# Kernel tuning notes

Measured on AMD Instinct MI355X. Metric: run time of the kernel, lower is better.

The kernel has to match this reference:

```python
import jax, jax.numpy as jnp
import numpy as np
from jax import lax

B, T, L = 16, 200, 250
IDIM, ODIM, DUNITS = 512, 80, 1024
ATT_DIM, ACONV_CHANS, ACONV_K = 128, 32, 31
PRENET = 256


def setup_inputs() -> dict:
    key = jax.random.key(0)
    ks = iter(jax.random.split(key, 40))
    def nrm(shape, fan_in):
        return jax.random.normal(next(ks), shape, jnp.float32) * (fan_in ** -0.5)
    inp = {}
    inp['hs'] = jax.random.normal(next(ks), (B, T, IDIM), jnp.float32)
    inp['hlens'] = jax.random.randint(next(ks), (B,), T // 2, T + 1)
    inp['ys'] = jax.random.normal(next(ks), (B, L, ODIM), jnp.float32)
    # location-aware attention params
    inp['W_enc'] = nrm((IDIM, ATT_DIM), IDIM)
    inp['b_enc'] = jnp.zeros((ATT_DIM,), jnp.float32)
    inp['W_dec'] = nrm((DUNITS, ATT_DIM), DUNITS)
    inp['W_att'] = nrm((ACONV_CHANS, ATT_DIM), ACONV_CHANS)
    inp['loc_conv_w'] = nrm((ACONV_CHANS, 1, ACONV_K), ACONV_K)
    inp['gvec_w'] = nrm((ATT_DIM,), ATT_DIM)
    inp['gvec_b'] = jnp.zeros((), jnp.float32)
    # prenet (no bias, dropout off in eval)
    inp['prenet_W1'] = nrm((ODIM, PRENET), ODIM)
    inp['prenet_W2'] = nrm((PRENET, PRENET), PRENET)
    # LSTM cells (torch gate order i,f,g,o; bih+bhh folded into one bias)
    in0 = IDIM + PRENET
    inp['Wih0'] = nrm((4 * DUNITS, in0), in0)
    inp['Whh0'] = nrm((4 * DUNITS, DUNITS), DUNITS)
    inp['b0'] = jnp.zeros((4 * DUNITS,), jnp.float32)
    inp['Wih1'] = nrm((4 * DUNITS, DUNITS), DUNITS)
    inp['Whh1'] = nrm((4 * DUNITS, DUNITS), DUNITS)
    inp['b1'] = jnp.zeros((4 * DUNITS,), jnp.float32)
    # output heads
    inp['feat_W'] = nrm((DUNITS, ODIM), DUNITS)
    inp['prob_W'] = nrm((DUNITS,), DUNITS)
    inp['prob_b'] = jnp.zeros((), jnp.float32)
    # postnet: conv(no bias) + BN(eval; running mean=0, var=1 folded away) + tanh
    inp['post_w_in'] = nrm((512, ODIM, 5), 5 * ODIM)
    inp['post_g_in'] = jnp.ones((512,), jnp.float32)
    inp['post_b_in'] = jnp.zeros((512,), jnp.float32)
    inp['post_w_mid'] = nrm((3, 512, 512, 5), 5 * 512)
    inp['post_g_mid'] = jnp.ones((3, 512), jnp.float32)
    inp['post_b_mid'] = jnp.zeros((3, 512), jnp.float32)
    inp['post_w_out'] = nrm((ODIM, 512, 5), 5 * 512)
    inp['post_g_out'] = jnp.ones((ODIM,), jnp.float32)
    inp['post_b_out'] = jnp.zeros((ODIM,), jnp.float32)
    return inp


def _conv1d(x, w, pad):
    # x: [B, Cin, T], w: [Cout, Cin, K]
    return lax.conv_general_dilated(x, w, (1,), [(pad, pad)],
                                    dimension_numbers=('NCH', 'OIH', 'NCH'))


def _lstm(x, h, c, Wih, Whh, b):
    g = x @ Wih.T + h @ Whh.T + b
    i, f, gg, o = jnp.split(g, 4, axis=-1)
    c2 = jax.nn.sigmoid(f) * c + jax.nn.sigmoid(i) * jnp.tanh(gg)
    return jax.nn.sigmoid(o) * jnp.tanh(c2), c2


def reference(hs, hlens, ys, W_enc, b_enc, W_dec, W_att, loc_conv_w, gvec_w, gvec_b,
              prenet_W1, prenet_W2, Wih0, Whh0, b0, Wih1, Whh1, b1,
              feat_W, prob_W, prob_b,
              post_w_in, post_g_in, post_b_in, post_w_mid, post_g_mid, post_b_mid,
              post_w_out, post_g_out, post_b_out):
    mask = jnp.arange(T)[None, :] < hlens[:, None]            # [B,T]
    pre_enc = hs @ W_enc + b_enc                              # [B,T,A] precomputed
    # teacher forcing: prenet input at step i is ys[:, i-1] (zeros at i=0);
    # prenet has no recurrent dependency -> vectorize over time
    prev = jnp.concatenate([jnp.zeros((B, 1, ODIM), hs.dtype), ys[:, :L - 1]], axis=1)
    pren = jax.nn.relu(jax.nn.relu(prev @ prenet_W1) @ prenet_W2)  # [B,L,256]
    att_w0 = mask.astype(hs.dtype) / hlens[:, None].astype(hs.dtype)
    z = jnp.zeros((B, DUNITS), hs.dtype)
    carry0 = (z, z, z, z, att_w0)

    def step(carry, pren_t):
        z0, c0, z1, c1, att_w = carry
        conv = _conv1d(att_w[:, None, :], loc_conv_w, ACONV_K // 2)   # [B,C,T]
        e = jnp.tanh(pre_enc + jnp.einsum('bct,ca->bta', conv, W_att)
                     + (z0 @ W_dec)[:, None, :]) @ gvec_w + gvec_b    # [B,T]
        e = jnp.where(mask, e, -1e30)
        w = jax.nn.softmax(2.0 * e, axis=1)                           # scaling=2.0
        att_c = jnp.einsum('bt,btd->bd', w, hs)
        x = jnp.concatenate([att_c, pren_t], axis=1)
        z0n, c0n = _lstm(x, z0, c0, Wih0, Whh0, b0)
        z1n, c1n = _lstm(z0n, z1, c1, Wih1, Whh1, b1)
        return (z0n, c0n, z1n, c1n, w), (z1n @ feat_W, z1n @ prob_W + prob_b)

    _, (outs, probs) = lax.scan(step, carry0, jnp.swapaxes(pren, 0, 1))
    outs = jnp.transpose(outs, (1, 2, 0))   # [B, odim, L] (matches torch.stack dim=2)
    probs = probs.T                         # [B, L]
    # postnet (BN in eval with running mean=0/var=1 reduces to gamma*x+beta)
    h = jnp.tanh(post_g_in[:, None] * _conv1d(outs, post_w_in, 2) + post_b_in[:, None])
    for i in range(3):
        h = jnp.tanh(post_g_mid[i][:, None] * _conv1d(h, post_w_mid[i], 2)
                     + post_b_mid[i][:, None])
    h = post_g_out[:, None] * _conv1d(h, post_w_out, 2) + post_b_out[:, None]
    post_outs = outs + h
    return jnp.swapaxes(post_outs, 1, 2), jnp.swapaxes(outs, 1, 2), probs
```

## Files before the change

### kernel.cpp

```cpp
#include <hip/hip_runtime.h>
#include <cstdint>
#include <cstddef>

constexpr int B_ = 16, T_ = 200, L_ = 250;
constexpr int IDIM = 512, ODIM = 80, DUNITS = 1024;
constexpr int ADIM = 128, ACH = 32, AK = 31;
constexpr int PRE = 256;
constexpr int TPAD = 208;

typedef _Float16 h16;
typedef _Float16 half8 __attribute__((ext_vector_type(8)));
typedef _Float16 half4 __attribute__((ext_vector_type(4)));
typedef float f32x4 __attribute__((ext_vector_type(4)));

constexpr int FSTEP = 800;
constexpr int FZ0W = 0, FDPW = 256, FAW = 288;

constexpr size_t OFF_PE    = 0;
constexpr size_t OFF_H0H   = 851968;
constexpr size_t OFF_Z1H   = 917504;
constexpr size_t OFF_ATTC  = 983040;
constexpr size_t OFF_DP    = 999424;
constexpr size_t OFF_FLAGS = 1007616;
constexpr size_t OFF_XT1   = 1807616;
constexpr size_t OFF_XTA   = 2888960;
constexpr size_t OFF_XTB   = 7214336;
constexpr size_t ZERO_BYTES= 11539712;
constexpr size_t OFF_MB    = 11539712;
constexpr size_t OFF_WDR   = 11547904;
constexpr size_t OFF_PREN  = 11810048;
constexpr size_t OFF_HSH   = 13858048;
constexpr size_t OFF_W0AH  = 17134848;
constexpr size_t OFF_WHH0  = 23426304;
constexpr size_t OFF_WI1   = 31814912;
constexpr size_t OFF_WHH1  = 40203520;
constexpr size_t OFF_Z1ALL = 48592128;
constexpr size_t OFF_WTIN  = 56784128;
constexpr size_t OFF_WTMID = 57439488;
constexpr size_t OFF_WTOUT = 65303808;
constexpr size_t OFF_PSC   = 65713408;

__device__ __forceinline__ float fsig(float x) {
  x = fminf(fmaxf(x, -30.f), 30.f);
  return __builtin_amdgcn_rcpf(1.f + __expf(-x));
}
__device__ __forceinline__ float ftanh(float x) {
  x = fminf(fmaxf(x, -15.f), 15.f);
  const float e = __expf(2.f * x);
  return (e - 1.f) * __builtin_amdgcn_rcpf(e + 1.f);
}
__device__ __forceinline__ f32x4 mfma16(half8 a, half8 b, f32x4 c) {
  return __builtin_amdgcn_mfma_f32_16x16x32_f16(a, b, c, 0, 0, 0);
}
__device__ __forceinline__ half8 load8_agent(const h16* p) {
  union { unsigned long long q[2]; half8 v; } cv;
  cv.q[0] = __hip_atomic_load((const unsigned long long*)p, __ATOMIC_RELAXED,
                              __HIP_MEMORY_SCOPE_AGENT);
  cv.q[1] = __hip_atomic_load(((const unsigned long long*)p) + 1, __ATOMIC_RELAXED,
                              __HIP_MEMORY_SCOPE_AGENT);
  return cv.v;
}
__device__ __forceinline__ float loadf_agent(const float* p) {
  union { unsigned u; float f; } cv;
  cv.u = __hip_atomic_load((const unsigned*)p, __ATOMIC_RELAXED,
                           __HIP_MEMORY_SCOPE_AGENT);
  return cv.f;
}
__device__ __forceinline__ void storef_agent(float* p, float v) {
  union { unsigned u; float f; } cv; cv.f = v;
  __hip_atomic_store((unsigned*)p, cv.u, __ATOMIC_RELAXED, __HIP_MEMORY_SCOPE_AGENT);
}
__device__ __forceinline__ int loadw(const int* p) {
  return __hip_atomic_load(p, __ATOMIC_RELAXED, __HIP_MEMORY_SCOPE_AGENT);
}
__device__ __forceinline__ void storew(int* p, int v) {
  __hip_atomic_store(p, v, __ATOMIC_RELAXED, __HIP_MEMORY_SCOPE_AGENT);
}
__device__ __forceinline__ void poll_n(const int* base, const int n) {
  if ((int)threadIdx.x < n) {
    const int* f = base + threadIdx.x;
    while (loadw(f) == 0) __builtin_amdgcn_s_sleep(1);
  }
  __syncthreads();
  __builtin_amdgcn_sched_barrier(0);
}
__device__ __forceinline__ void poll_all256(const int* base) {
  const int* f = base + threadIdx.x;
  while (loadw(f) == 0) __builtin_amdgcn_s_sleep(1);
  __syncthreads();
  __builtin_amdgcn_sched_barrier(0);
}


__global__ void k_zero(float4* __restrict__ p, int n4) {
  const int i = blockIdx.x * blockDim.x + threadIdx.x;
  if (i < n4) p[i] = make_float4(0.f, 0.f, 0.f, 0.f);
}

__global__ void __launch_bounds__(128) k_preenc(const float* __restrict__ hs,
    const float* __restrict__ W_enc, const float* __restrict__ b_enc,
    h16* __restrict__ pe_h) {
  const int bt = blockIdx.x, b = bt / T_, tt = bt % T_;
  __shared__ float s[IDIM];
  for (int i = threadIdx.x; i < IDIM; i += 128) s[i] = hs[(size_t)bt * IDIM + i];
  __syncthreads();
  const int a = threadIdx.x;
  float acc = b_enc[a];
#pragma unroll 4
  for (int d = 0; d < IDIM; ++d) acc += s[d] * W_enc[d * ADIM + a];
  pe_h[((size_t)b * ADIM + a) * TPAD + tt] = (h16)acc;
}

__global__ void k_precMb(const float* __restrict__ lconv, const float* __restrict__ W_att,
                         h16* __restrict__ Mb) {
  const int at = blockIdx.x, lane = threadIdx.x;
  const int a = at * 16 + (lane & 15);
  const int k0 = (lane >> 4) * 8;
  half8 o;
#pragma unroll
  for (int j = 0; j < 8; ++j) {
    const int k = k0 + j;
    float v = 0.f;
    if (k < AK)
      for (int c = 0; c < ACH; ++c) v += lconv[c * AK + k] * W_att[c * ADIM + a];
    o[j] = (h16)v;
  }
  *(half8*)(Mb + (size_t)(at * 64 + lane) * 8) = o;
}

__global__ void k_cvt_perm(const float* __restrict__ src, h16* __restrict__ dst,
                           const int K) {
  const int rr = blockIdx.x;
  const int u = rr >> 2, g = rr & 3;
  const float* s = src + (size_t)(g * 1024 + u) * K;
  h16* d = dst + (size_t)rr * K;
  for (int k = threadIdx.x; k < K; k += 256) d[k] = (h16)s[k];
}

__global__ void k_cvt_wdec(const float* __restrict__ Wdec, h16* __restrict__ Wdr) {
  const int a = blockIdx.x;
  for (int k = threadIdx.x; k < 1024; k += 256)
    Wdr[(size_t)a * 1024 + k] = (h16)Wdec[(size_t)k * ADIM + a];
}

__global__ void k_cvt_f32f16(const float* __restrict__ src, h16* __restrict__ dst) {
  const size_t i = ((size_t)blockIdx.x * 256 + threadIdx.x) * 4;
  const float4 v = *(const float4*)(src + i);
  half4 o; o[0] = (h16)v.x; o[1] = (h16)v.y; o[2] = (h16)v.z; o[3] = (h16)v.w;
  *(half4*)(dst + i) = o;
}

__global__ void k_prenet1(const float* __restrict__ ys, const float* __restrict__ W1,
                          float* __restrict__ h1) {
  const int bl = blockIdx.x, b = bl / L_, l = bl % L_;
  __shared__ float s[ODIM];
  if (threadIdx.x < ODIM)
    s[threadIdx.x] = (l == 0) ? 0.f : ys[((size_t)b * L_ + l - 1) * ODIM + threadIdx.x];
  __syncthreads();
  const int p = threadIdx.x;
  float acc = 0.f;
#pragma unroll 4
  for (int o = 0; o < ODIM; ++o) acc += s[o] * W1[o * PRE + p];
  h1[(size_t)bl * PRE + p] = fmaxf(acc, 0.f);
}

__global__ void k_prenet2h(const float* __restrict__ h1, const float* __restrict__ W2,
                           h16* __restrict__ pren_h) {
  const int bl = blockIdx.x, b = bl / L_, ll = bl % L_;
  __shared__ float s[PRE];
  s[threadIdx.x] = h1[(size_t)bl * PRE + threadIdx.x];
  __syncthreads();
  const int p = threadIdx.x;
  float acc = 0.f;
#pragma unroll 4
  for (int o = 0; o < PRE; ++o) acc += s[o] * W2[o * PRE + p];
  pren_h[((size_t)ll * B_ + b) * PRE + p] = (h16)fmaxf(acc, 0.f);
}

__global__ void k_cvt_wpin(const float* __restrict__ w, h16* __restrict__ o) {
  const int co = blockIdx.x;
  for (int i = threadIdx.x; i < 640; i += 256) {
    const int k = i >> 7, ci = i & 127;
    o[(size_t)co * 640 + i] = (ci < 80) ? (h16)w[((size_t)co * 80 + ci) * 5 + k] : (h16)0.f;
  }
}
__global__ void k_cvt_wpmid(const float* __restrict__ w, h16* __restrict__ o) {
  const int idx = blockIdx.x;
  const float* s = w + (size_t)idx * 512 * 5;
  h16* d = o + (size_t)idx * 2560;
  for (int i = threadIdx.x; i < 2560; i += 256) {
    const int k = i >> 9, ci = i & 511;
    d[i] = (h16)s[(size_t)ci * 5 + k];
  }
}
__global__ void k_cvt_wpout(const float* __restrict__ w, h16* __restrict__ o) {
  const int co = blockIdx.x;
  for (int i = threadIdx.x; i < 2560; i += 256) {
    const int k = i >> 9, ci = i & 511;
    o[(size_t)co * 2560 + i] = (h16)w[((size_t)co * 512 + ci) * 5 + k];
  }
}

template <int CIP, int NK, bool TANH, bool FINAL>
__global__ void __launch_bounds__(256) k_cvmf(const h16* __restrict__ xT,
    const h16* __restrict__ wT, const float* __restrict__ gamma,
    const float* __restrict__ beta, h16* __restrict__ yT,
    const float* __restrict__ res, float* __restrict__ out0) {
  __shared__ float s_red[4][64][5];
  __shared__ float s_g[16][20];
  constexpr int KTOT = NK * 128;
  const int b = blockIdx.x, l0 = blockIdx.y * 16, co0 = blockIdx.z * 16;
  const int tid = threadIdx.x, lane = tid & 63, wave = tid >> 6;
  const int nloc = lane & 15, kl8 = (lane >> 4) * 8;
  const h16* wr = wT + (size_t)(co0 + nloc) * KTOT + wave * (NK * 32) + kl8;
  half8 w[NK];
#pragma unroll
  for (int c = 0; c < NK; ++c) w[c] = *(const half8*)(wr + c * 32);
  f32x4 acc = {0.f, 0.f, 0.f, 0.f};
  const h16* xb = xT + (size_t)b * 264 * CIP;
#pragma unroll
  for (int c = 0; c < NK; ++c) {
    const int kg = wave * (NK * 32) + c * 32;
    const int k = kg / CIP, ci = kg & (CIP - 1);
    const half8 a = *(const half8*)(xb + (size_t)(l0 + nloc + k) * CIP + ci + kl8);
    acc = mfma16(a, w[c], acc);
  }
#pragma unroll
  for (int r = 0; r < 4; ++r) s_red[wave][lane][r] = acc[r];
  __syncthreads();
  {
    const float v = s_red[0][lane][wave] + s_red[1][lane][wave]
                  + s_red[2][lane][wave] + s_red[3][lane][wave];
    s_g[lane & 15][4 * (lane >> 4) + wave] = v;
  }
  __syncthreads();
  {
    const int co_l = tid & 15, l_l = tid >> 4;
    const int co = co0 + co_l, l = l0 + l_l;
    if (l < L_) {
      float v = gamma[co] * s_g[co_l][l_l] + beta[co];
      if (TANH) v = ftanh(v);
      if (FINAL) {
        const size_t o = ((size_t)b * L_ + l) * ODIM + co;
        out0[o] = res[o] + v;
      } else {
        yT[((size_t)b * 264 + l + 2) * 512 + co] = (h16)v;
      }
    }
  }
}


struct ScanP {
  const h16 *pe_h, *Mb, *Wdr, *hs_h, *pren_h;
  const h16 *W0ah, *Whh0h, *Wz01h, *Whh1h;
  h16 *h0h, *z1h, *attc;
  float *dp;
  const float *gvw, *b0, *b1;
  const int *hlens;
  h16 *z1all;
  int *flags;
};

__device__ __forceinline__ void lstm0_partA(const h16* pren_t, const h16* z0p,
    const half8 wA[6], const half8 wH[8], f32x4& acc) {
  const int lane = threadIdx.x & 63, wave = threadIdx.x >> 6;
  const int nloc = lane & 15, kl8 = (lane >> 4) * 8;
  half8 rz[8];
#pragma unroll
  for (int c = 0; c < 8; ++c)
    rz[c] = load8_agent(z0p + nloc * DUNITS + wave * 256 + c * 32 + kl8);
#pragma unroll
  for (int c = 0; c < 8; ++c) acc = mfma16(rz[c], wH[c], acc);
#pragma unroll
  for (int c = 0; c < 6; ++c) {
    const int kg = wave * 192 + c * 32;
    if (kg >= 512)
      acc = mfma16(*(const half8*)(pren_t + nloc * PRE + (kg - 512) + kl8), wA[c], acc);
  }
}

__device__ __forceinline__ void lstm0_partB(const ScanP& P,
    h16* z0o, const int slab, const half8 wA[6], float& c0reg, f32x4 acc,
    float sred[4][64][5], float sg[16][20], h16* sho) {
  const int tid = threadIdx.x;
  const int lane = tid & 63, wave = tid >> 6;
  const int nloc = lane & 15, kl8 = (lane >> 4) * 8;
  half8 ra[6];
#pragma unroll
  for (int c = 0; c < 6; ++c) {
    const int kg = wave * 192 + c * 32;
    if (kg < 512) ra[c] = load8_agent(P.attc + nloc * IDIM + kg + kl8);
  }
#pragma unroll
  for (int c = 0; c < 6; ++c) {
    const int kg = wave * 192 + c * 32;
    if (kg < 512) acc = mfma16(ra[c], wA[c], acc);
  }
#pragma unroll
  for (int r = 0; r < 4; ++r) sred[wave][lane][r] = acc[r];
  __syncthreads();
  {
    const float v = sred[0][lane][wave] + sred[1][lane][wave]
                  + sred[2][lane][wave] + sred[3][lane][wave];
    sg[lane & 15][4 * (lane >> 4) + wave] = v;
  }
  __syncthreads();
  if (tid < 64) {
    const int ul = tid >> 4, b = tid & 15;
    const int u = slab * 4 + ul;
    const float xi = sg[ul * 4 + 0][b] + P.b0[u];
    const float xf = sg[ul * 4 + 1][b] + P.b0[1024 + u];
    const float xg = sg[ul * 4 + 2][b] + P.b0[2048 + u];
    const float xo = sg[ul * 4 + 3][b] + P.b0[3072 + u];
    const float cn = fsig(xf) * c0reg + fsig(xi) * ftanh(xg);
    c0reg = cn;
    sho[ul * 16 + b] = (h16)(fsig(xo) * ftanh(cn));
  }
  __syncthreads();
  if (tid < 16) {
    union { h16 h[4]; unsigned long long q; } u4;
#pragma unroll
    for (int j = 0; j < 4; ++j) u4.h[j] = sho[j * 16 + tid];
    __hip_atomic_store((unsigned long long*)(z0o + tid * DUNITS + slab * 4), u4.q,
                       __ATOMIC_RELAXED, __HIP_MEMORY_SCOPE_AGENT);
  }
}

__device__ __forceinline__ void lstm1_mm(const ScanP& P, const half8 r0[8],
    const half8 r1[8], h16* z1o, h16* z1all_s, const int slab,
    const half8 wI[8], const half8 wHH[8], float& c1reg,
    float sred[4][64][5], float sg[16][20], h16* sho) {
  const int tid = threadIdx.x;
  const int lane = tid & 63, wave = tid >> 6;
  f32x4 acc = {0.f, 0.f, 0.f, 0.f};
#pragma unroll
  for (int c = 0; c < 8; ++c) acc = mfma16(r0[c], wI[c], acc);
#pragma unroll
  for (int c = 0; c < 8; ++c) acc = mfma16(r1[c], wHH[c], acc);
#pragma unroll
  for (int r = 0; r < 4; ++r) sred[wave][lane][r] = acc[r];
  __syncthreads();
  {
    const float v = sred[0][lane][wave] + sred[1][lane][wave]
                  + sred[2][lane][wave] + sred[3][lane][wave];
    sg[lane & 15][4 * (lane >> 4) + wave] = v;
  }
  __syncthreads();
  if (tid < 64) {
    const int ul = tid >> 4, b = tid & 15;
    const int u = slab * 4 + ul;
    const float xi = sg[ul * 4 + 0][b] + P.b1[u];
    const float xf = sg[ul * 4 + 1][b] + P.b1[1024 + u];
    const float xg = sg[ul * 4 + 2][b] + P.b1[2048 + u];
    const float xo = sg[ul * 4 + 3][b] + P.b1[3072 + u];
    const float cn = fsig(xf) * c1reg + fsig(xi) * ftanh(xg);
    c1reg = cn;
    const float hn = fsig(xo) * ftanh(cn);
    const h16 hh = (h16)hn;
    z1all_s[b * DUNITS + u] = hh;
    sho[ul * 16 + b] = hh;
  }
  __syncthreads();
  if (tid < 16) {
    union { h16 h[4]; unsigned long long q; } u4;
#pragma unroll
    for (int j = 0; j < 4; ++j) u4.h[j] = sho[j * 16 + tid];
    __hip_atomic_store((unsigned long long*)(z1o + tid * DUNITS + slab * 4), u4.q,
                       __ATOMIC_RELAXED, __HIP_MEMORY_SCOPE_AGENT);
  }
}

__global__ void __launch_bounds__(256, 1) k_scan(const ScanP P) {
  __shared__ float s_red[4][64][5];
  __shared__ float s_g[16][20];
  __shared__ h16   s_ho[64];
  __shared__ float s_aw[240];
  __shared__ float s_dp[ADIM];
  __shared__ float s_gv[ADIM];
  __shared__ float s_ew[256];
  __shared__ float s_wt[208];
  __shared__ float s_par[4][512];
  __shared__ float s_r8[8];
  __shared__ float s_bc[2];
  __shared__ float s_cvpe[13][8][64][4];

  const int blk = blockIdx.x, tid = threadIdx.x;
  const int lane = tid & 63, wave = tid >> 6;
  constexpr int BD = B_ * DUNITS;

  if (blk < 16) {
    const int b = blk;
    const int hl = P.hlens[b];
    const int mtmax = (hl + 15) >> 4;
    const int slab = 240 + b;
    const int l15 = lane & 15;
    half8 bfrag[8];
#pragma unroll
    for (int at = 0; at < 8; ++at)
      bfrag[at] = *(const half8*)(P.Mb + (size_t)(at * 64 + lane) * 8);
    half8 wA[6], wH[8];
    {
      const int nloc = lane & 15, kl8 = (lane >> 4) * 8;
      const h16* wrA = P.W0ah + ((size_t)(slab * 16 + nloc)) * 768 + wave * 192 + kl8;
      const h16* wrH = P.Whh0h + ((size_t)(slab * 16 + nloc)) * 1024 + wave * 256 + kl8;
#pragma unroll
      for (int c = 0; c < 6; ++c) wA[c] = *(const half8*)(wrA + c * 32);
#pragma unroll
      for (int c = 0; c < 8; ++c) wH[c] = *(const half8*)(wrH + c * 32);
    }
    if (tid < 240) {
      const int tt = tid - 15;
      s_aw[tid] = (tt >= 0 && tt < hl) ? (1.f / (float)hl) : 0.f;
    }
    if (tid < ADIM) s_gv[tid] = P.gvw[tid];
    __syncthreads();
    float c0reg = 0.f;

    for (int mi = 0; mi < 4; ++mi) {
      const int mt = wave + mi * 4;
      if (mt < mtmax) {
        half8 af;
#pragma unroll
        for (int j = 0; j < 8; ++j)
          af[j] = (h16)s_aw[mt * 16 + l15 + (lane >> 4) * 8 + j];
        const int t0 = mt * 16 + 4 * (lane >> 4);
        half4 pe[8];
#pragma unroll
        for (int at = 0; at < 8; ++at)
          pe[at] = *(const half4*)(P.pe_h + ((size_t)b * ADIM + at * 16 + l15) * TPAD + t0);
#pragma unroll
        for (int at = 0; at < 8; ++at) {
          f32x4 z4 = {0.f, 0.f, 0.f, 0.f};
          const f32x4 cv = mfma16(af, bfrag[at], z4);
          float4 o;
          o.x = cv[0] + (float)pe[at][0]; o.y = cv[1] + (float)pe[at][1];
          o.z = cv[2] + (float)pe[at][2]; o.w = cv[3] + (float)pe[at][3];
          *(float4*)&s_cvpe[mt][at][lane][0] = o;
        }
      }
    }
    __syncthreads();

    for (int i = 0; i < L_; ++i) {
      const h16* z0p = P.h0h + (size_t)(i & 1) * BD;
      h16* z0o = P.h0h + (size_t)((i & 1) ^ 1) * BD;
      int* sf = P.flags + (size_t)i * FSTEP;
      poll_n(sf + FDPW, 8);
      if (tid < ADIM) s_dp[tid] = loadf_agent(P.dp + b * ADIM + tid);
      __syncthreads();
#pragma unroll
      for (int mi = 0; mi < 4; ++mi) {
        const int mt = wave + mi * 4;
        if (mt < mtmax) {
          const int t0 = mt * 16 + 4 * (lane >> 4);
          float e0 = 0.f, e1 = 0.f, e2 = 0.f, e3 = 0.f;
#pragma unroll
          for (int at = 0; at < 8; ++at) {
            const float4 v = *(const float4*)&s_cvpe[mt][at][lane][0];
            const int a = at * 16 + l15;
            const float g = s_gv[a], d = s_dp[a];
            e0 += g * ftanh(v.x + d);
            e1 += g * ftanh(v.y + d);
            e2 += g * ftanh(v.z + d);
            e3 += g * ftanh(v.w + d);
          }
#pragma unroll
          for (int o = 1; o < 16; o <<= 1) {
            e0 += __shfl_xor(e0, o); e1 += __shfl_xor(e1, o);
            e2 += __shfl_xor(e2, o); e3 += __shfl_xor(e3, o);
          }
          if (l15 == 0) {
            s_ew[t0 + 0] = e0; s_ew[t0 + 1] = e1; s_ew[t0 + 2] = e2; s_ew[t0 + 3] = e3;
          }
        }
      }
      __syncthreads();
      const float val = (tid < hl) ? 2.f * s_ew[tid] : -3.0e38f;
      float m = val;
#pragma unroll
      for (int o = 32; o > 0; o >>= 1) m = fmaxf(m, __shfl_xor(m, o));
      if ((tid & 63) == 0) s_r8[tid >> 6] = m;
      __syncthreads();
      if (tid == 0) s_bc[0] = fmaxf(fmaxf(s_r8[0], s_r8[1]), fmaxf(s_r8[2], s_r8[3]));
      __syncthreads();
      const float pp = (tid < hl) ? __expf(val - s_bc[0]) : 0.f;
      float ssum = pp;
#pragma unroll
      for (int o = 32; o > 0; o >>= 1) ssum += __shfl_xor(ssum, o);
      if ((tid & 63) == 0) s_r8[4 + (tid >> 6)] = ssum;
      __syncthreads();
      if (tid == 0) s_bc[1] = __builtin_amdgcn_rcpf(s_r8[4] + s_r8[5] + s_r8[6] + s_r8[7]);
      __syncthreads();
      if (tid < T_) {
        const float w = pp * s_bc[1];
        s_wt[tid] = w;
        s_aw[15 + tid] = w;
      }
      __syncthreads();
      const h16* hsb = P.hs_h + (size_t)b * T_ * IDIM;
      {
        const int d0 = lane * 8;
        const h16* hp = hsb + d0;
        float a8[8] = {0.f, 0.f, 0.f, 0.f, 0.f, 0.f, 0.f, 0.f};
        int tt = wave;
        for (; tt + 12 < hl; tt += 16) {
          const half8 h0 = *(const half8*)(hp + (size_t)tt * IDIM);
          const half8 h1 = *(const half8*)(hp + (size_t)(tt + 4) * IDIM);
          const half8 h2 = *(const half8*)(hp + (size_t)(tt + 8) * IDIM);
          const half8 h3 = *(const half8*)(hp + (size_t)(tt + 12) * IDIM);
          const float w0 = s_wt[tt], w1 = s_wt[tt + 4];
          const float w2 = s_wt[tt + 8], w3 = s_wt[tt + 12];
#pragma unroll
          for (int j = 0; j < 8; ++j)
            a8[j] += w0 * (float)h0[j] + w1 * (float)h1[j]
                   + w2 * (float)h2[j] + w3 * (float)h3[j];
        }
        for (; tt < hl; tt += 4) {
          const half8 hv = *(const half8*)(hp + (size_t)tt * IDIM);
          const float wt = s_wt[tt];
#pragma unroll
          for (int j = 0; j < 8; ++j) a8[j] += wt * (float)hv[j];
        }
#pragma unroll
        for (int j = 0; j < 8; ++j) s_par[wave][d0 + j] = a8[j];
      }
      __syncthreads();
      {
        const int d = tid * 2;
        const float cx0 = s_par[0][d] + s_par[1][d] + s_par[2][d] + s_par[3][d];
        const float cx1 = s_par[0][d + 1] + s_par[1][d + 1] + s_par[2][d + 1]
                        + s_par[3][d + 1];
        union { h16 h[2]; unsigned u; } cv;
        cv.h[0] = (h16)cx0; cv.h[1] = (h16)cx1;
        __hip_atomic_store((unsigned*)(P.attc + b * IDIM + d), cv.u,
                           __ATOMIC_RELAXED, __HIP_MEMORY_SCOPE_AGENT);
      }
      asm volatile("s_waitcnt vmcnt(0)" ::: "memory");
      __syncthreads();
      if (tid < 16) storew(sf + FAW + tid * 32 + b, 1);
      f32x4 acc0 = {0.f, 0.f, 0.f, 0.f};
      lstm0_partA(P.pren_h + (size_t)i * (B_ * PRE), z0p, wA, wH, acc0);
      poll_n(sf + FAW + (blk & 15) * 32, 16);
      lstm0_partB(P, z0o, slab, wA, c0reg, acc0, s_red, s_g, s_ho);
      asm volatile("s_waitcnt vmcnt(0)" ::: "memory");
      __syncthreads();
      if (tid == 0) storew(sf + FZ0W + blk, 1);
      for (int mi = 0; mi < 4; ++mi) {
        const int mt = wave + mi * 4;
        if (mt < mtmax) {
          half8 af;
#pragma unroll
          for (int j = 0; j < 8; ++j)
            af[j] = (h16)s_aw[mt * 16 + l15 + (lane >> 4) * 8 + j];
          const int t0 = mt * 16 + 4 * (lane >> 4);
          half4 pe[8];
#pragma unroll
          for (int at = 0; at < 8; ++at)
            pe[at] = *(const half4*)(P.pe_h + ((size_t)b * ADIM + at * 16 + l15) * TPAD + t0);
#pragma unroll
          for (int at = 0; at < 8; ++at) {
            f32x4 z4 = {0.f, 0.f, 0.f, 0.f};
            const f32x4 cv = mfma16(af, bfrag[at], z4);
            float4 o;
            o.x = cv[0] + (float)pe[at][0]; o.y = cv[1] + (float)pe[at][1];
            o.z = cv[2] + (float)pe[at][2]; o.w = cv[3] + (float)pe[at][3];
            *(float4*)&s_cvpe[mt][at][lane][0] = o;
          }
        }
      }
      __syncthreads();
    }
    return;
  }

  const int g = blk - 16;
  const bool dbl = (g < 16);
  const bool isdp = (g >= 16 && g < 24);
  half8 wA0[6], wH0[8], wI1a[8], wHH1a[8], wI1b[8], wHH1b[8], wD[8];
  {
    const int nloc = lane & 15, kl8 = (lane >> 4) * 8;
    const h16* wrA = P.W0ah + ((size_t)(g * 16 + nloc)) * 768 + wave * 192 + kl8;
    const h16* wrH = P.Whh0h + ((size_t)(g * 16 + nloc)) * 1024 + wave * 256 + kl8;
    const h16* wrI = P.Wz01h + ((size_t)(g * 16 + nloc)) * 1024 + wave * 256 + kl8;
    const h16* wrX = P.Whh1h + ((size_t)(g * 16 + nloc)) * 1024 + wave * 256 + kl8;
#pragma unroll
    for (int c = 0; c < 6; ++c) wA0[c] = *(const half8*)(wrA + c * 32);
#pragma unroll
    for (int c = 0; c < 8; ++c) wH0[c] = *(const half8*)(wrH + c * 32);
#pragma unroll
    for (int c = 0; c < 8; ++c) wI1a[c] = *(const half8*)(wrI + c * 32);
#pragma unroll
    for (int c = 0; c < 8; ++c) wHH1a[c] = *(const half8*)(wrX + c * 32);
    if (dbl) {
      const h16* wrI2 = P.Wz01h + ((size_t)((240 + g) * 16 + nloc)) * 1024 + wave * 256 + kl8;
      const h16* wrX2 = P.Whh1h + ((size_t)((240 + g) * 16 + nloc)) * 1024 + wave * 256 + kl8;
#pragma unroll
      for (int c = 0; c < 8; ++c) wI1b[c] = *(const half8*)(wrI2 + c * 32);
#pragma unroll
      for (int c = 0; c < 8; ++c) wHH1b[c] = *(const half8*)(wrX2 + c * 32);
    }
    if (isdp) {
      const h16* wrD = P.Wdr + ((size_t)((g - 16) * 16 + nloc)) * 1024 + wave * 256 + kl8;
#pragma unroll
      for (int c = 0; c < 8; ++c) wD[c] = *(const half8*)(wrD + c * 32);
    }
  }
  float c0reg = 0.f, c1a = 0.f, c1b = 0.f;
  const int nloc = lane & 15, kl8 = (lane >> 4) * 8;

  for (int i = 0; i < L_; ++i) {
    const h16* z0p = P.h0h + (size_t)(i & 1) * BD;
    h16* z0o = P.h0h + (size_t)((i & 1) ^ 1) * BD;
    const h16* z1p = P.z1h + (size_t)((i & 1) ^ 1) * BD;
    h16* z1o = P.z1h + (size_t)(i & 1) * BD;
    int* sf = P.flags + (size_t)i * FSTEP;
    if (i > 0) poll_all256(P.flags + (size_t)(i - 1) * FSTEP + FZ0W);
    if (isdp) {
      half8 rz[8];
#pragma unroll
      for (int c = 0; c < 8; ++c)
        rz[c] = load8_agent(z0p + nloc * DUNITS + wave * 256 + c * 32 + kl8);
      f32x4 acc = {0.f, 0.f, 0.f, 0.f};
#pragma unroll
      for (int c = 0; c < 8; ++c) acc = mfma16(rz[c], wD[c], acc);
#pragma unroll
      for (int r = 0; r < 4; ++r) s_red[wave][lane][r] = acc[r];
      __syncthreads();
      {
        const float v = s_red[0][lane][wave] + s_red[1][lane][wave]
                      + s_red[2][lane][wave] + s_red[3][lane][wave];
        const int row = lane & 15, batch = 4 * (lane >> 4) + wave;
        storef_agent(P.dp + batch * ADIM + (g - 16) * 16 + row, v);
      }
      asm volatile("s_waitcnt vmcnt(0)" ::: "memory");
      __syncthreads();
      if (tid == 0) storew(sf + FDPW + (g - 16), 1);
    }
    if (i > 0) {
      half8 r0[8], r1[8];
#pragma unroll
      for (int c = 0; c < 8; ++c)
        r0[c] = load8_agent(z0p + nloc * DUNITS + wave * 256 + c * 32 + kl8);
#pragma unroll
      for (int c = 0; c < 8; ++c)
        r1[c] = load8_agent(z1p + nloc * DUNITS + wave * 256 + c * 32 + kl8);
      h16* z1s = P.z1all + (size_t)(i - 1) * BD;
      lstm1_mm(P, r0, r1, z1o, z1s, g, wI1a, wHH1a, c1a, s_red, s_g, s_ho);
      if (dbl)
        lstm1_mm(P, r0, r1, z1o, z1s, 240 + g, wI1b, wHH1b, c1b, s_red, s_g, s_ho);
    }
    f32x4 acc0 = {0.f, 0.f, 0.f, 0.f};
    lstm0_partA(P.pren_h + (size_t)i * (B_ * PRE), z0p, wA0, wH0, acc0);
    poll_n(sf + FAW + (blk & 15) * 32, 16);
    lstm0_partB(P, z0o, g, wA0, c0reg, acc0, s_red, s_g, s_ho);
    asm volatile("s_waitcnt vmcnt(0)" ::: "memory");
    __syncthreads();
    if (tid == 0) storew(sf + FZ0W + blk, 1);
  }
  poll_all256(P.flags + (size_t)(L_ - 1) * FSTEP + FZ0W);
  {
    const h16* z0p = P.h0h + (size_t)(L_ & 1) * BD;
    const h16* z1p = P.z1h + (size_t)((L_ & 1) ^ 1) * BD;
    h16* z1o = P.z1h + (size_t)(L_ & 1) * BD;
    h16* z1s = P.z1all + (size_t)(L_ - 1) * BD;
    half8 r0[8], r1[8];
#pragma unroll
    for (int c = 0; c < 8; ++c)
      r0[c] = load8_agent(z0p + nloc * DUNITS + wave * 256 + c * 32 + kl8);
#pragma unroll
    for (int c = 0; c < 8; ++c)
      r1[c] = load8_agent(z1p + nloc * DUNITS + wave * 256 + c * 32 + kl8);
    lstm1_mm(P, r0, r1, z1o, z1s, g, wI1a, wHH1a, c1a, s_red, s_g, s_ho);
    if (dbl)
      lstm1_mm(P, r0, r1, z1o, z1s, 240 + g, wI1b, wHH1b, c1b, s_red, s_g, s_ho);
  }
}


__global__ void __launch_bounds__(128) k_heads(const h16* __restrict__ z1_all,
    const float* __restrict__ feat_W, const float* __restrict__ prob_W,
    const float* __restrict__ prob_b, float* __restrict__ out1,
    float* __restrict__ probs, h16* __restrict__ xT1) {
  const int bl = blockIdx.x, b = bl / L_, l = bl % L_;
  __shared__ float s_z[DUNITS];
  const h16* z = z1_all + ((size_t)l * B_ + b) * DUNITS;
  for (int i = threadIdx.x; i < DUNITS; i += 128) s_z[i] = (float)z[i];
  __syncthreads();
  const int co = threadIdx.x;
  if (co < ODIM) {
    float acc = 0.f;
#pragma unroll 4
    for (int d = 0; d < DUNITS; ++d) acc += s_z[d] * feat_W[d * ODIM + co];
    out1[((size_t)b * L_ + l) * ODIM + co] = acc;
    xT1[((size_t)b * 264 + l + 2) * 128 + co] = (h16)acc;
  } else if (co == 96) {
    float acc = prob_b[0];
#pragma unroll 4
    for (int d = 0; d < DUNITS; ++d) acc += s_z[d] * prob_W[d];
    probs[(size_t)b * L_ + l] = acc;
  }
}


extern "C" void kernel_launch(void* const* d_in, const int* in_sizes, int n_in,
                              void* d_out, int out_size, void* d_ws, size_t ws_size,
                              hipStream_t stream) {
  const float* hs    = (const float*)d_in[0];
  const int*   hlens = (const int*)d_in[1];
  const float* ys    = (const float*)d_in[2];
  const float* W_enc = (const float*)d_in[3];
  const float* b_enc = (const float*)d_in[4];
  const float* W_dec = (const float*)d_in[5];
  const float* W_att = (const float*)d_in[6];
  const float* lconv = (const float*)d_in[7];
  const float* gvw   = (const float*)d_in[8];
  const float* pW1   = (const float*)d_in[10];
  const float* pW2   = (const float*)d_in[11];
  const float* Wih0  = (const float*)d_in[12];
  const float* Whh0  = (const float*)d_in[13];
  const float* b0    = (const float*)d_in[14];
  const float* Wih1  = (const float*)d_in[15];
  const float* Whh1  = (const float*)d_in[16];
  const float* b1    = (const float*)d_in[17];
  const float* featW = (const float*)d_in[18];
  const float* probW = (const float*)d_in[19];
  const float* probB = (const float*)d_in[20];
  const float* pwin  = (const float*)d_in[21];
  const float* pgin  = (const float*)d_in[22];
  const float* pbin  = (const float*)d_in[23];
  const float* pwmid = (const float*)d_in[24];
  const float* pgmid = (const float*)d_in[25];
  const float* pbmid = (const float*)d_in[26];
  const float* pwout = (const float*)d_in[27];
  const float* pgout = (const float*)d_in[28];
  const float* pbout = (const float*)d_in[29];

  char* ws = (char*)d_ws;
  h16*   pe_h   = (h16*)(ws + OFF_PE);
  h16*   h0h    = (h16*)(ws + OFF_H0H);
  h16*   z1h    = (h16*)(ws + OFF_Z1H);
  h16*   attc_h = (h16*)(ws + OFF_ATTC);
  float* dp     = (float*)(ws + OFF_DP);
  int*   flags  = (int*)(ws + OFF_FLAGS);
  h16*   xT1    = (h16*)(ws + OFF_XT1);
  h16*   xTA    = (h16*)(ws + OFF_XTA);
  h16*   xTB    = (h16*)(ws + OFF_XTB);
  h16*   Mb     = (h16*)(ws + OFF_MB);
  h16*   Wdr    = (h16*)(ws + OFF_WDR);
  h16*   pren_h = (h16*)(ws + OFF_PREN);
  h16*   hs_h   = (h16*)(ws + OFF_HSH);
  h16*   W0ah   = (h16*)(ws + OFF_W0AH);
  h16*   Whh0h  = (h16*)(ws + OFF_WHH0);
  h16*   Wz01h  = (h16*)(ws + OFF_WI1);
  h16*   Whh1h  = (h16*)(ws + OFF_WHH1);
  h16*   z1all  = (h16*)(ws + OFF_Z1ALL);
  h16*   wTin   = (h16*)(ws + OFF_WTIN);
  h16*   wTmid  = (h16*)(ws + OFF_WTMID);
  h16*   wTout  = (h16*)(ws + OFF_WTOUT);
  float* psc    = (float*)(ws + OFF_PSC);

  float* out0 = (float*)d_out;
  float* out1 = out0 + (size_t)B_ * L_ * ODIM;
  float* out2 = out1 + (size_t)B_ * L_ * ODIM;

  hipLaunchKernelGGL(k_zero, dim3((ZERO_BYTES / 16 + 255) / 256), dim3(256), 0, stream,
                     (float4*)ws, (int)(ZERO_BYTES / 16));
  hipLaunchKernelGGL(k_preenc, dim3(B_ * T_), dim3(128), 0, stream, hs, W_enc, b_enc, pe_h);
  hipLaunchKernelGGL(k_precMb, dim3(8), dim3(64), 0, stream, lconv, W_att, Mb);
  hipLaunchKernelGGL(k_cvt_perm, dim3(4096), dim3(256), 0, stream, Wih0, W0ah, 768);
  hipLaunchKernelGGL(k_cvt_perm, dim3(4096), dim3(256), 0, stream, Whh0, Whh0h, 1024);
  hipLaunchKernelGGL(k_cvt_perm, dim3(4096), dim3(256), 0, stream, Wih1, Wz01h, 1024);
  hipLaunchKernelGGL(k_cvt_perm, dim3(4096), dim3(256), 0, stream, Whh1, Whh1h, 1024);
  hipLaunchKernelGGL(k_cvt_wdec, dim3(128), dim3(256), 0, stream, W_dec, Wdr);
  hipLaunchKernelGGL(k_cvt_f32f16, dim3(1600), dim3(256), 0, stream, hs, hs_h);
  hipLaunchKernelGGL(k_prenet1, dim3(B_ * L_), dim3(PRE), 0, stream, ys, pW1, psc);
  hipLaunchKernelGGL(k_prenet2h, dim3(B_ * L_), dim3(PRE), 0, stream, psc, pW2, pren_h);
  hipLaunchKernelGGL(k_cvt_wpin, dim3(512), dim3(256), 0, stream, pwin, wTin);
  hipLaunchKernelGGL(k_cvt_wpmid, dim3(3 * 512), dim3(256), 0, stream, pwmid, wTmid);
  hipLaunchKernelGGL(k_cvt_wpout, dim3(80), dim3(256), 0, stream, pwout, wTout);

  ScanP S{pe_h, Mb, Wdr, hs_h, pren_h, W0ah, Whh0h, Wz01h, Whh1h,
          h0h, z1h, attc_h, dp, gvw, b0, b1, hlens, z1all, flags};
  hipLaunchKernelGGL(k_scan, dim3(256), dim3(256), 0, stream, S);

  hipLaunchKernelGGL(k_heads, dim3(B_ * L_), dim3(128), 0, stream,
                     z1all, featW, probW, probB, out1, out2, xT1);

  hipLaunchKernelGGL((k_cvmf<128, 5, true, false>), dim3(16, 16, 32), dim3(256), 0, stream,
                     xT1, wTin, pgin, pbin, xTA, nullptr, nullptr);
  hipLaunchKernelGGL((k_cvmf<512, 20, true, false>), dim3(16, 16, 32), dim3(256), 0, stream,
                     xTA, wTmid, pgmid, pbmid, xTB, nullptr, nullptr);
  hipLaunchKernelGGL((k_cvmf<512, 20, true, false>), dim3(16, 16, 32), dim3(256), 0, stream,
                     xTB, wTmid + (size_t)512 * 2560, pgmid + 512, pbmid + 512,
                     xTA, nullptr, nullptr);
  hipLaunchKernelGGL((k_cvmf<512, 20, true, false>), dim3(16, 16, 32), dim3(256), 0, stream,
                     xTA, wTmid + (size_t)2 * 512 * 2560, pgmid + 1024, pbmid + 1024,
                     xTB, nullptr, nullptr);
  hipLaunchKernelGGL((k_cvmf<512, 20, false, true>), dim3(16, 16, 5), dim3(256), 0, stream,
                     xTB, wTout, pgout, pbout, nullptr, out1, out0);
}
```

Measured before the change: 6.101 ms.

## Replace scalar prenet, encoder projection and output heads with fp16 MFMA GEMMs

Swaps the scalar FMA kernels for the encoder projection, the two prenet layers and the feature/prob heads for one templated fp16 MFMA GEMM kernel with per-use epilogues. It adds small conversion kernels that transpose and pad the weights and decoder inputs into fp16 K-contiguous layouts. The aim is to cut the time spent outside the recurrent scan by using matrix cores in place of per-thread dot products. In exchange the prenet hidden layer and head inputs are now computed in fp16, which costs some precision, and several small prep launches are added.

```diff
diff --git a/kernel.cpp b/kernel.cpp
--- a/kernel.cpp
+++ b/kernel.cpp
@@ -38,7 +38,12 @@
 constexpr size_t OFF_WTIN  = 56784128;
 constexpr size_t OFF_WTMID = 57439488;
 constexpr size_t OFF_WTOUT = 65303808;
-constexpr size_t OFF_PSC   = 65713408;
+constexpr size_t OFF_YSP   = 65713408;
+constexpr size_t OFF_H1P   = 66481408;
+constexpr size_t OFF_W1P   = 68529408;
+constexpr size_t OFF_W2P   = 68578560;
+constexpr size_t OFF_WENCP = 68709632;
+constexpr size_t OFF_FWP   = 68840704;
 
 __device__ __forceinline__ float fsig(float x) {
   x = fminf(fmaxf(x, -30.f), 30.f);
@@ -97,20 +102,6 @@
   if (i < n4) p[i] = make_float4(0.f, 0.f, 0.f, 0.f);
 }
 
-__global__ void __launch_bounds__(128) k_preenc(const float* __restrict__ hs,
-    const float* __restrict__ W_enc, const float* __restrict__ b_enc,
-    h16* __restrict__ pe_h) {
-  const int bt = blockIdx.x, b = bt / T_, tt = bt % T_;
-  __shared__ float s[IDIM];
-  for (int i = threadIdx.x; i < IDIM; i += 128) s[i] = hs[(size_t)bt * IDIM + i];
-  __syncthreads();
-  const int a = threadIdx.x;
-  float acc = b_enc[a];
-#pragma unroll 4
-  for (int d = 0; d < IDIM; ++d) acc += s[d] * W_enc[d * ADIM + a];
-  pe_h[((size_t)b * ADIM + a) * TPAD + tt] = (h16)acc;
-}
-
 __global__ void k_precMb(const float* __restrict__ lconv, const float* __restrict__ W_att,
                          h16* __restrict__ Mb) {
   const int at = blockIdx.x, lane = threadIdx.x;
@@ -150,33 +141,6 @@
   *(half4*)(dst + i) = o;
 }
 
-__global__ void k_prenet1(const float* __restrict__ ys, const float* __restrict__ W1,
-                          float* __restrict__ h1) {
-  const int bl = blockIdx.x, b = bl / L_, l = bl % L_;
-  __shared__ float s[ODIM];
-  if (threadIdx.x < ODIM)
-    s[threadIdx.x] = (l == 0) ? 0.f : ys[((size_t)b * L_ + l - 1) * ODIM + threadIdx.x];
-  __syncthreads();
-  const int p = threadIdx.x;
-  float acc = 0.f;
-#pragma unroll 4
-  for (int o = 0; o < ODIM; ++o) acc += s[o] * W1[o * PRE + p];
-  h1[(size_t)bl * PRE + p] = fmaxf(acc, 0.f);
-}
-
-__global__ void k_prenet2h(const float* __restrict__ h1, const float* __restrict__ W2,
-                           h16* __restrict__ pren_h) {
-  const int bl = blockIdx.x, b = bl / L_, ll = bl % L_;
-  __shared__ float s[PRE];
-  s[threadIdx.x] = h1[(size_t)bl * PRE + threadIdx.x];
-  __syncthreads();
-  const int p = threadIdx.x;
-  float acc = 0.f;
-#pragma unroll 4
-  for (int o = 0; o < PRE; ++o) acc += s[o] * W2[o * PRE + p];
-  pren_h[((size_t)ll * B_ + b) * PRE + p] = (h16)fmaxf(acc, 0.f);
-}
-
 __global__ void k_cvt_wpin(const float* __restrict__ w, h16* __restrict__ o) {
   const int co = blockIdx.x;
   for (int i = threadIdx.x; i < 640; i += 256) {
@@ -198,6 +162,79 @@
   for (int i = threadIdx.x; i < 2560; i += 256) {
     const int k = i >> 9, ci = i & 511;
     o[(size_t)co * 2560 + i] = (h16)w[((size_t)co * 512 + ci) * 5 + k];
+  }
+}
+
+__global__ void k_p_ys(const float* __restrict__ ys, h16* __restrict__ ysp) {
+  const int m = blockIdx.x;
+  const int l = m >> 4, b = m & 15;
+  const int co = threadIdx.x;
+  h16 v = (h16)0.f;
+  if (l > 0 && co < 80) v = (h16)ys[((size_t)b * L_ + (l - 1)) * ODIM + co];
+  ysp[(size_t)m * 96 + co] = v;
+}
+__global__ void k_p_w1(const float* __restrict__ W1, h16* __restrict__ W1p) {
+  const int p = blockIdx.x;
+  const int o = threadIdx.x;
+  W1p[(size_t)p * 96 + o] = (o < 80) ? (h16)W1[(size_t)o * PRE + p] : (h16)0.f;
+}
+__global__ void k_p_w2(const float* __restrict__ W2, h16* __restrict__ W2p) {
+  const int p2 = blockIdx.x;
+  const int p = threadIdx.x;
+  W2p[(size_t)p2 * 256 + p] = (h16)W2[(size_t)p * PRE + p2];
+}
+__global__ void k_p_wenc(const float* __restrict__ We, h16* __restrict__ Wp) {
+  const int a = blockIdx.x;
+  for (int d = threadIdx.x; d < 512; d += 256)
+    Wp[(size_t)a * 512 + d] = (h16)We[(size_t)d * ADIM + a];
+}
+__global__ void k_p_fw(const float* __restrict__ fw, const float* __restrict__ pw,
+                       h16* __restrict__ Wp) {
+  const int co = blockIdx.x;
+  for (int d = threadIdx.x; d < 1024; d += 256) {
+    h16 v = (h16)0.f;
+    if (co < 80) v = (h16)fw[(size_t)d * ODIM + co];
+    else if (co == 80) v = (h16)pw[d];
+    Wp[(size_t)co * 1024 + d] = v;
+  }
+}
+
+template <int KCH, int EPI>
+__global__ void __launch_bounds__(256) k_gemw(const h16* __restrict__ A,
+    const h16* __restrict__ W, h16* __restrict__ dsth, float* __restrict__ dstf,
+    float* __restrict__ dstf2, const float* __restrict__ bvec) {
+  constexpr int KA = KCH * 32;
+  const int m0 = blockIdx.x * 16, n0 = blockIdx.y * 64;
+  const int lane = threadIdx.x & 63, wave = threadIdx.x >> 6;
+  const int nloc = lane & 15, kl8 = (lane >> 4) * 8;
+  const h16* wr = W + (size_t)(n0 + wave * 16 + nloc) * KA + kl8;
+  half8 w[KCH];
+#pragma unroll
+  for (int c = 0; c < KCH; ++c) w[c] = *(const half8*)(wr + c * 32);
+  const h16* ar = A + (size_t)(m0 + nloc) * KA + kl8;
+  f32x4 acc = {0.f, 0.f, 0.f, 0.f};
+#pragma unroll
+  for (int c = 0; c < KCH; ++c)
+    acc = mfma16(*(const half8*)(ar + c * 32), w[c], acc);
+  const int n = n0 + wave * 16 + (lane & 15);
+#pragma unroll
+  for (int r = 0; r < 4; ++r) {
+    const int m = m0 + 4 * (lane >> 4) + r;
+    const float v = acc[r];
+    if (EPI == 0) {
+      dsth[(size_t)m * 256 + n] = (h16)fmaxf(v, 0.f);
+    } else if (EPI == 1) {
+      const int b = m / 200, t = m % 200;
+      dsth[((size_t)b * 128 + n) * TPAD + t] = (h16)(v + bvec[n]);
+    } else {
+      const int b = m & 15, l = m >> 4;
+      if (n < 80) {
+        dstf[((size_t)b * L_ + l) * ODIM + n] = v;
+        dsth[((size_t)b * 264 + l + 2) * 128 + n] = (h16)v;
+      } else if (n == 80) {
+        dstf2[(size_t)b * L_ + l] = v + bvec[0];
+      }
+    }
   }
 }
 
@@ -674,31 +711,6 @@
     lstm1_mm(P, r0, r1, z1o, z1s, g, wI1a, wHH1a, c1a, s_red, s_g, s_ho);
     if (dbl)
       lstm1_mm(P, r0, r1, z1o, z1s, 240 + g, wI1b, wHH1b, c1b, s_red, s_g, s_ho);
-  }
-}
-
-
-__global__ void __launch_bounds__(128) k_heads(const h16* __restrict__ z1_all,
-    const float* __restrict__ feat_W, const float* __restrict__ prob_W,
-    const float* __restrict__ prob_b, float* __restrict__ out1,
-    float* __restrict__ probs, h16* __restrict__ xT1) {
-  const int bl = blockIdx.x, b = bl / L_, l = bl % L_;
-  __shared__ float s_z[DUNITS];
-  const h16* z = z1_all + ((size_t)l * B_ + b) * DUNITS;
-  for (int i = threadIdx.x; i < DUNITS; i += 128) s_z[i] = (float)z[i];
-  __syncthreads();
-  const int co = threadIdx.x;
-  if (co < ODIM) {
-    float acc = 0.f;
-#pragma unroll 4
-    for (int d = 0; d < DUNITS; ++d) acc += s_z[d] * feat_W[d * ODIM + co];
-    out1[((size_t)b * L_ + l) * ODIM + co] = acc;
-    xT1[((size_t)b * 264 + l + 2) * 128 + co] = (h16)acc;
-  } else if (co == 96) {
-    float acc = prob_b[0];
-#pragma unroll 4
-    for (int d = 0; d < DUNITS; ++d) acc += s_z[d] * prob_W[d];
-    probs[(size_t)b * L_ + l] = acc;
   }
 }
 
@@ -758,7 +770,12 @@
   h16*   wTin   = (h16*)(ws + OFF_WTIN);
   h16*   wTmid  = (h16*)(ws + OFF_WTMID);
   h16*   wTout  = (h16*)(ws + OFF_WTOUT);
-  float* psc    = (float*)(ws + OFF_PSC);
+  h16*   ysp    = (h16*)(ws + OFF_YSP);
+  h16*   h1p    = (h16*)(ws + OFF_H1P);
+  h16*   W1p    = (h16*)(ws + OFF_W1P);
+  h16*   W2p    = (h16*)(ws + OFF_W2P);
+  h16*   Wencp  = (h16*)(ws + OFF_WENCP);
+  h16*   featWp = (h16*)(ws + OFF_FWP);
 
   float* out0 = (float*)d_out;
   float* out1 = out0 + (size_t)B_ * L_ * ODIM;
@@ -766,7 +783,6 @@
 
   hipLaunchKernelGGL(k_zero, dim3((ZERO_BYTES / 16 + 255) / 256), dim3(256), 0, stream,
                      (float4*)ws, (int)(ZERO_BYTES / 16));
-  hipLaunchKernelGGL(k_preenc, dim3(B_ * T_), dim3(128), 0, stream, hs, W_enc, b_enc, pe_h);
   hipLaunchKernelGGL(k_precMb, dim3(8), dim3(64), 0, stream, lconv, W_att, Mb);
   hipLaunchKernelGGL(k_cvt_perm, dim3(4096), dim3(256), 0, stream, Wih0, W0ah, 768);
   hipLaunchKernelGGL(k_cvt_perm, dim3(4096), dim3(256), 0, stream, Whh0, Whh0h, 1024);
@@ -774,18 +790,28 @@
   hipLaunchKernelGGL(k_cvt_perm, dim3(4096), dim3(256), 0, stream, Whh1, Whh1h, 1024);
   hipLaunchKernelGGL(k_cvt_wdec, dim3(128), dim3(256), 0, stream, W_dec, Wdr);
   hipLaunchKernelGGL(k_cvt_f32f16, dim3(1600), dim3(256), 0, stream, hs, hs_h);
-  hipLaunchKernelGGL(k_prenet1, dim3(B_ * L_), dim3(PRE), 0, stream, ys, pW1, psc);
-  hipLaunchKernelGGL(k_prenet2h, dim3(B_ * L_), dim3(PRE), 0, stream, psc, pW2, pren_h);
   hipLaunchKernelGGL(k_cvt_wpin, dim3(512), dim3(256), 0, stream, pwin, wTin);
   hipLaunchKernelGGL(k_cvt_wpmid, dim3(3 * 512), dim3(256), 0, stream, pwmid, wTmid);
   hipLaunchKernelGGL(k_cvt_wpout, dim3(80), dim3(256), 0, stream, pwout, wTout);
+  hipLaunchKernelGGL(k_p_ys, dim3(4000), dim3(96), 0, stream, ys, ysp);
+  hipLaunchKernelGGL(k_p_w1, dim3(256), dim3(96), 0, stream, pW1, W1p);
+  hipLaunchKernelGGL(k_p_w2, dim3(256), dim3(256), 0, stream, pW2, W2p);
+  hipLaunchKernelGGL(k_p_wenc, dim3(128), dim3(256), 0, stream, W_enc, Wencp);
+  hipLaunchKernelGGL(k_p_fw, dim3(128), dim3(256), 0, stream, featW, probW, featWp);
+
+  hipLaunchKernelGGL((k_gemw<16, 1>), dim3(200, 2), dim3(256), 0, stream,
+                     hs_h, Wencp, pe_h, nullptr, nullptr, b_enc);
+  hipLaunchKernelGGL((k_gemw<3, 0>), dim3(250, 4), dim3(256), 0, stream,
+                     ysp, W1p, h1p, nullptr, nullptr, nullptr);
+  hipLaunchKernelGGL((k_gemw<8, 0>), dim3(250, 4), dim3(256), 0, stream,
+                     h1p, W2p, pren_h, nullptr, nullptr, nullptr);
 
   ScanP S{pe_h, Mb, Wdr, hs_h, pren_h, W0ah, Whh0h, Wz01h, Whh1h,
           h0h, z1h, attc_h, dp, gvw, b0, b1, hlens, z1all, flags};
   hipLaunchKernelGGL(k_scan, dim3(256), dim3(256), 0, stream, S);
 
-  hipLaunchKernelGGL(k_heads, dim3(B_ * L_), dim3(128), 0, stream,
-                     z1all, featW, probW, probB, out1, out2, xT1);
+  hipLaunchKernelGGL((k_gemw<32, 2>), dim3(250, 2), dim3(256), 0, stream,
+                     z1all, featWp, xT1, out1, out2, probB);
 
   hipLaunchKernelGGL((k_cvmf<128, 5, true, false>), dim3(16, 16, 32), dim3(256), 0, stream,
                      xT1, wTin, pgin, pbin, xTA, nullptr, nullptr);
```

After: 5.977 ms. -2.0%, faster.
